# Optimization experiments

Measured on AMD Instinct MI355X. Metric: run time of the kernel, lower is better.

The kernel has to match this reference:

```python
import jax, jax.numpy as jnp
import numpy as np
import math

B, N, D_IN, D_OUT = 8, 2048, 128, 128
NEG_BIG = -10000.0

def setup_inputs() -> dict:
    key = jax.random.key(0)
    k_in, k_adj, kq, kk, kv, kbq, kbk, kbv = jax.random.split(key, 8)
    scale = 1.0 / math.sqrt(D_IN)
    inputs = jax.random.normal(k_in, (B, N, D_IN), dtype=jnp.float32)
    adj = jax.random.randint(k_adj, (B, N, N), 0, 2, dtype=jnp.int32)
    Wq = jax.random.uniform(kq, (D_IN, D_OUT), jnp.float32, -scale, scale)
    Wk = jax.random.uniform(kk, (D_IN, D_OUT), jnp.float32, -scale, scale)
    Wv = jax.random.uniform(kv, (D_IN, D_OUT), jnp.float32, -scale, scale)
    bq = jax.random.uniform(kbq, (D_OUT,), jnp.float32, -scale, scale)
    bk = jax.random.uniform(kbk, (D_OUT,), jnp.float32, -scale, scale)
    bv = jax.random.uniform(kbv, (D_OUT,), jnp.float32, -scale, scale)
    return {"inputs": inputs, "adj": adj, "Wq": Wq, "bq": bq,
            "Wk": Wk, "bk": bk, "Wv": Wv, "bv": bv}

def reference(inputs, adj, Wq, bq, Wk, bk, Wv, bv):
    # QKV projections: [B, N, D_OUT]
    q = inputs @ Wq + bq
    k = inputs @ Wk + bk
    v = inputs @ Wv + bv
    # additive adjacency bias: 0 where edge, -10000 where no edge
    bias = (1.0 - adj.astype(jnp.float32)) * NEG_BIG
    # scaled dot-product scores [B, N, N]
    a = jnp.einsum('bnd,bmd->bnm', q, k) / jnp.sqrt(jnp.float32(q.shape[-1]))
    a = a + bias
    p = jax.nn.softmax(a, axis=-1)  # dropout_prob=0.0 -> identity
    h = jnp.einsum('bnm,bmd->bnd', p, v)
    return jax.nn.elu(h)
```

## Files before the change

### kernel.cpp

```cpp
#include <hip/hip_runtime.h>

typedef unsigned short u16;
typedef __bf16 bf16x8 __attribute__((ext_vector_type(8)));
typedef float  fx4    __attribute__((ext_vector_type(4)));

__device__ __forceinline__ u16 f2bf(float f) {
    unsigned int x = __builtin_bit_cast(unsigned int, f);
    x = x + 0x7fffu + ((x >> 16) & 1u);
    return (u16)(x >> 16);
}
__device__ __forceinline__ __bf16 f2bf16(float f) {
    return __builtin_bit_cast(__bf16, f2bf(f));
}
__device__ __forceinline__ u16 f2bf_fast(float f) {
    return __builtin_bit_cast(u16, (__bf16)f);
}
__device__ __forceinline__ float exp2_fast(float x) {
#if __has_builtin(__builtin_amdgcn_exp2f)
    return __builtin_amdgcn_exp2f(x);
#else
    float r;
    __asm__ volatile("v_exp_f32 %0, %1" : "=v"(r) : "v"(x));
    return r;
#endif
}
__device__ __forceinline__ int ld_nt(const int* p) {
    return __builtin_nontemporal_load(p);
}

#define MFMA16(a, b, c) __builtin_amdgcn_mfma_f32_16x16x32_bf16((a), (b), (c), 0, 0, 0)
#define WAVE_LDS_SYNC() __asm__ volatile("s_waitcnt lgkmcnt(0)" ::: "memory")

__global__ __launch_bounds__(256) void wt_kernel(
    const float* __restrict__ Wq, const float* __restrict__ Wk,
    const float* __restrict__ Wv, u16* __restrict__ WT)
{
    const int o = blockIdx.x * 256 + threadIdx.x;
    const int p = o >> 14, rem = o & 16383, c = rem >> 7, k = rem & 127;
    const float* W = (p == 0) ? Wq : ((p == 1) ? Wk : Wv);
    WT[o] = f2bf(W[k * 128 + c]);
}

__global__ __launch_bounds__(256, 2) void qkv_kernel(
    const float* __restrict__ X, const u16* __restrict__ WT,
    const float* __restrict__ bq, const float* __restrict__ bk,
    const float* __restrict__ bv,
    u16* __restrict__ Qf, u16* __restrict__ Kf, u16* __restrict__ Vf)
{
    __shared__ __align__(16) u16 st[4][1024];

    const int tid  = threadIdx.x;
    const int w    = tid >> 6;
    const int lane = tid & 63;
    const int n    = lane & 15;
    const int quad = lane >> 4;
    const int gw   = blockIdx.x * 4 + w;
    const int rt   = gw >> 1, ch = gw & 1;
    const int row0 = rt * 16;
    const int b    = row0 >> 11;
    const int keyb = row0 & 2047;

    u16* sw = st[w];

    bf16x8 af[4];
    {
        const float* xr = X + (size_t)(row0 + n) * 128;
#pragma unroll
        for (int kk = 0; kk < 4; ++kk) {
            float4 f0 = *(const float4*)(xr + kk * 32 + quad * 8);
            float4 f1 = *(const float4*)(xr + kk * 32 + quad * 8 + 4);
            bf16x8 a;
            a[0] = f2bf16(f0.x); a[1] = f2bf16(f0.y); a[2] = f2bf16(f0.z); a[3] = f2bf16(f0.w);
            a[4] = f2bf16(f1.x); a[5] = f2bf16(f1.y); a[6] = f2bf16(f1.z); a[7] = f2bf16(f1.w);
            af[kk] = a;
        }
    }

    const float* Bs[2] = {bq, bk};
#pragma unroll
    for (int p = 0; p < 2; ++p) {
        const u16* wt = WT + p * 16384;
#pragma unroll
        for (int nt = 0; nt < 4; ++nt) {
            const int col0 = ch * 64 + nt * 16;
            fx4 acc = {0.f, 0.f, 0.f, 0.f};
#pragma unroll
            for (int kk = 0; kk < 4; ++kk) {
                bf16x8 bf = __builtin_bit_cast(bf16x8,
                    *(const uint4*)&wt[(col0 + n) * 128 + kk * 32 + quad * 8]);
                acc = MFMA16(af[kk], bf, acc);
            }
            const float bb = Bs[p][col0 + n];
            const int c = col0 + n;
            const int li = ((c >> 5) & 1) * 512 + ((c >> 3) & 3) * 128 + (c & 7);
#pragma unroll
            for (int r = 0; r < 4; ++r)
                sw[li + (quad * 4 + r) * 8] = f2bf(acc[r] + bb);
        }
        WAVE_LDS_SYNC();
        u16* gbase;
        if (p == 0) {
            gbase = Qf + (((size_t)(b * 128 + (keyb >> 4)) * 4 + 2 * ch) << 9);
        } else {
            gbase = Kf + (((size_t)((b * 64 + (keyb >> 5)) * 2 + ((keyb >> 4) & 1)) * 4 + 2 * ch) << 9);
        }
        *(uint4*)(gbase + lane * 8)       = *(const uint4*)(sw + lane * 8);
        *(uint4*)(gbase + 512 + lane * 8) = *(const uint4*)(sw + 512 + lane * 8);
    }

    {
        const u16* wtv = WT + 2 * 16384;
        const int hk    = (keyb >> 4) & 1;
        const int vtile = keyb >> 5;
#pragma unroll
        for (int d0 = 0; d0 < 4; ++d0) {
            const int dbase = ch * 64 + d0 * 16;
            fx4 acc = {0.f, 0.f, 0.f, 0.f};
#pragma unroll
            for (int kk = 0; kk < 4; ++kk) {
                bf16x8 wf = __builtin_bit_cast(bf16x8,
                    *(const uint4*)&wtv[(dbase + n) * 128 + kk * 32 + quad * 8]);
                acc = MFMA16(wf, af[kk], acc);
            }
            const int li = d0 * 256 + ((n >> 3) & 1) * 128 + (n & 7);
#pragma unroll
            for (int r = 0; r < 4; ++r)
                sw[li + (quad * 4 + r) * 8] = f2bf(acc[r] + bv[dbase + quad * 4 + r]);
        }
        WAVE_LDS_SYNC();
        const int l5 = lane >> 5, lo = lane & 31;
#pragma unroll
        for (int i = 0; i < 2; ++i) {
            const int c2 = l5 + 2 * i;
            u16* g = Vf + (((size_t)(b * 64 + vtile) * 8 + ch * 4 + c2) << 9)
                        + hk * 256 + lo * 8;
            *(uint4*)g = *(const uint4*)(sw + c2 * 256 + lo * 8);
        }
    }
}

__global__ __launch_bounds__(256, 3) void attn_kernel(
    const u16* __restrict__ Qf, const u16* __restrict__ Kf,
    const u16* __restrict__ Vf, const int* __restrict__ adj,
    float* __restrict__ out)
{
    __shared__ __align__(16) float mO[4][16 * 128];
    __shared__ __align__(16) float ml[4][16];
    __shared__ __align__(16) u16 pl[4][640];

    const int tid  = threadIdx.x;
    const int h    = tid >> 6;
    const int lane = tid & 63;
    const int n    = lane & 15;
    const int quad = lane >> 4;
    const int b    = blockIdx.x & 7;
    const int qt   = blockIdx.x >> 3;
    const int q0   = qt * 16;
    const size_t bN = (size_t)b * 2048;

    bf16x8 qf[4];
    {
        const u16* qp = Qf + ((size_t)(b * 128 + qt) << 11) + lane * 8;
#pragma unroll
        for (int kk = 0; kk < 4; ++kk)
            qf[kk] = __builtin_bit_cast(bf16x8, *(const uint4*)(qp + (kk << 9)));
    }
    const u16* Kb = Kf + ((size_t)b << 18);
    const u16* Vb = Vf + ((size_t)b << 18);

    fx4 O[8];
#pragma unroll
    for (int i = 0; i < 8; ++i) O[i] = (fx4){0.f, 0.f, 0.f, 0.f};
    fx4 Lacc = {0.f, 0.f, 0.f, 0.f};

    bf16x8 ONESF;
    {
        const __bf16 one = __builtin_bit_cast(__bf16, (u16)0x3F80);
#pragma unroll
        for (int j = 0; j < 8; ++j) ONESF[j] = one;
    }

    const int* adjb = adj + (bN + q0 + quad * 4) * 2048;
    const float C2 = 0.12751742f;
    const float MB = -14427.0f;
    u16* pw = pl[h];

    float b0c[4], b1c[4];
    {
        const int k0 = h * 512;
#pragma unroll
        for (int r = 0; r < 4; ++r) {
            b0c[r] = ld_nt(&adjb[(size_t)r * 2048 + k0 + n])      ? 0.f : MB;
            b1c[r] = ld_nt(&adjb[(size_t)r * 2048 + k0 + 16 + n]) ? 0.f : MB;
        }
    }

    for (int t = 0; t < 16; ++t) {
        const int tg = h * 16 + t;
        const u16* kt_ = Kb + ((size_t)tg << 12) + lane * 8;
        const u16* vt_ = Vb + ((size_t)tg << 12) + lane * 8;

        bf16x8 kb[8];
#pragma unroll
        for (int kk = 0; kk < 8; ++kk)
            kb[kk] = __builtin_bit_cast(bf16x8, *(const uint4*)(kt_ + (kk << 9)));

        bf16x8 vf[8];
#pragma unroll
        for (int dt = 0; dt < 8; ++dt)
            vf[dt] = __builtin_bit_cast(bf16x8, *(const uint4*)(vt_ + (dt << 9)));

        float b0n[4], b1n[4];
        if (t < 15) {
            const int kn = h * 512 + (t + 1) * 32;
#pragma unroll
            for (int r = 0; r < 4; ++r) {
                b0n[r] = ld_nt(&adjb[(size_t)r * 2048 + kn + n])      ? 0.f : MB;
                b1n[r] = ld_nt(&adjb[(size_t)r * 2048 + kn + 16 + n]) ? 0.f : MB;
            }
        }

        fx4 S0 = {0.f, 0.f, 0.f, 0.f}, S1 = {0.f, 0.f, 0.f, 0.f};
#pragma unroll
        for (int kk = 0; kk < 4; ++kk) {
            S0 = MFMA16(qf[kk], kb[kk], S0);
            S1 = MFMA16(qf[kk], kb[4 + kk], S1);
        }

#pragma unroll
        for (int r = 0; r < 4; ++r) {
            const float e0 = exp2_fast(__builtin_fmaf(S0[r], C2, b0c[r]));
            const float e1 = exp2_fast(__builtin_fmaf(S1[r], C2, b1c[r]));
            pw[(quad * 4 + r) * 40 + n]      = f2bf_fast(e0);
            pw[(quad * 4 + r) * 40 + 16 + n] = f2bf_fast(e1);
        }

        WAVE_LDS_SYNC();
        bf16x8 pf = __builtin_bit_cast(bf16x8, *(const uint4*)&pw[n * 40 + quad * 8]);

#pragma unroll
        for (int dt = 0; dt < 8; ++dt)
            O[dt] = MFMA16(pf, vf[dt], O[dt]);
        Lacc = MFMA16(pf, ONESF, Lacc);

#pragma unroll
        for (int r = 0; r < 4; ++r) { b0c[r] = b0n[r]; b1c[r] = b1n[r]; }
    }

#pragma unroll
    for (int r = 0; r < 4; ++r) {
        const int row = quad * 4 + r;
        if (n == 0) ml[h][row] = Lacc[r];
#pragma unroll
        for (int dt = 0; dt < 8; ++dt)
            mO[h][row * 128 + dt * 16 + n] = O[dt][r];
    }
    __syncthreads();

#pragma unroll
    for (int r = 0; r < 4; ++r) {
        const int row = quad * 4 + r;
        const float L = ml[0][row] + ml[1][row] + ml[2][row] + ml[3][row];
        const float linv = 1.f / L;
        float* po = out + (bN + q0 + row) * 128;
#pragma unroll
        for (int dti = 0; dti < 2; ++dti) {
            const int dt = h * 2 + dti;
            float o = 0.f;
#pragma unroll
            for (int g = 0; g < 4; ++g) o += mO[g][row * 128 + dt * 16 + n];
            const float hh = o * linv;
            po[dt * 16 + n] = (hh > 0.f) ? hh : (__expf(hh) - 1.f);
        }
    }
}

extern "C" void kernel_launch(void* const* d_in, const int* in_sizes, int n_in,
                              void* d_out, int out_size, void* d_ws, size_t ws_size,
                              hipStream_t stream) {
    (void)in_sizes; (void)n_in; (void)out_size; (void)ws_size;
    const float* X   = (const float*)d_in[0];
    const int*   adj = (const int*)d_in[1];
    const float* Wq  = (const float*)d_in[2];
    const float* bq  = (const float*)d_in[3];
    const float* Wk  = (const float*)d_in[4];
    const float* bk  = (const float*)d_in[5];
    const float* Wv  = (const float*)d_in[6];
    const float* bv  = (const float*)d_in[7];
    float* out = (float*)d_out;

    u16* WT  = (u16*)d_out;
    u16* Qf  = (u16*)d_ws;
    u16* Kf  = Qf + (size_t)16384 * 128;
    u16* Vf  = Kf + (size_t)16384 * 128;

    wt_kernel<<<192, 256, 0, stream>>>(Wq, Wk, Wv, WT);
    qkv_kernel<<<512, 256, 0, stream>>>(X, WT, bq, bk, bv, Qf, Kf, Vf);
    attn_kernel<<<1024, 256, 0, stream>>>(Qf, Kf, Vf, adj, out);
}
```

Before: 302.8 us.

## Pre-pack adjacency into bitmask kernel and read bits in attention

Adds a pack kernel that uses wave ballots to compress the int32 adjacency matrix into a 64-bit-per-64-entries bitmask in workspace. The attention kernel then loads one 32-bit mask word per row per tile instead of 32 int32 values, and raises its occupancy launch bound from 3 to 4. The adjacency still has to be read once in full by the pack kernel, so the main saving is fewer loads and less register pressure inside the attention loop, at the cost of an extra launch and a small mask write and read.

```diff
diff --git a/kernel.cpp b/kernel.cpp
--- a/kernel.cpp
+++ b/kernel.cpp
@@ -1,6 +1,8 @@
 #include <hip/hip_runtime.h>
 
 typedef unsigned short u16;
+typedef unsigned int   u32;
+typedef unsigned long long u64;
 typedef __bf16 bf16x8 __attribute__((ext_vector_type(8)));
 typedef float  fx4    __attribute__((ext_vector_type(4)));
 
@@ -39,6 +41,25 @@
     const int p = o >> 14, rem = o & 16383, c = rem >> 7, k = rem & 127;
     const float* W = (p == 0) ? Wq : ((p == 1) ? Wk : Wv);
     WT[o] = f2bf(W[k * 128 + c]);
+}
+
+__global__ __launch_bounds__(256) void pack_kernel(
+    const int* __restrict__ adj, u64* __restrict__ mask64)
+{
+    const int w = threadIdx.x >> 6, lane = threadIdx.x & 63;
+    const int gw = blockIdx.x * 4 + w;
+    const int nw = gridDim.x * 4;
+    for (int it = gw; it < 131072; it += nw) {
+        const int* base = adj + (size_t)it * 256 + lane;
+        const u64 b0 = __ballot(ld_nt(base +   0) != 0);
+        const u64 b1 = __ballot(ld_nt(base +  64) != 0);
+        const u64 b2 = __ballot(ld_nt(base + 128) != 0);
+        const u64 b3 = __ballot(ld_nt(base + 192) != 0);
+        if (lane < 4) {
+            const u64 v = (lane == 0) ? b0 : (lane == 1) ? b1 : (lane == 2) ? b2 : b3;
+            mask64[(size_t)it * 4 + lane] = v;
+        }
+    }
 }
 
 __global__ __launch_bounds__(256, 2) void qkv_kernel(
@@ -139,9 +160,9 @@
     }
 }
 
-__global__ __launch_bounds__(256, 3) void attn_kernel(
+__global__ __launch_bounds__(256, 4) void attn_kernel(
     const u16* __restrict__ Qf, const u16* __restrict__ Kf,
-    const u16* __restrict__ Vf, const int* __restrict__ adj,
+    const u16* __restrict__ Vf, const u32* __restrict__ mask,
     float* __restrict__ out)
 {
     __shared__ __align__(16) float mO[4][16 * 128];
@@ -180,20 +201,14 @@
         for (int j = 0; j < 8; ++j) ONESF[j] = one;
     }
 
-    const int* adjb = adj + (bN + q0 + quad * 4) * 2048;
+    const u32* mrow = mask + (bN + q0 + quad * 4) * 64 + h * 16;
     const float C2 = 0.12751742f;
     const float MB = -14427.0f;
     u16* pw = pl[h];
 
-    float b0c[4], b1c[4];
-    {
-        const int k0 = h * 512;
-#pragma unroll
-        for (int r = 0; r < 4; ++r) {
-            b0c[r] = ld_nt(&adjb[(size_t)r * 2048 + k0 + n])      ? 0.f : MB;
-            b1c[r] = ld_nt(&adjb[(size_t)r * 2048 + k0 + 16 + n]) ? 0.f : MB;
-        }
-    }
+    u32 mc[4];
+#pragma unroll
+    for (int r = 0; r < 4; ++r) mc[r] = mrow[r * 64];
 
     for (int t = 0; t < 16; ++t) {
         const int tg = h * 16 + t;
@@ -210,14 +225,10 @@
         for (int dt = 0; dt < 8; ++dt)
             vf[dt] = __builtin_bit_cast(bf16x8, *(const uint4*)(vt_ + (dt << 9)));
 
-        float b0n[4], b1n[4];
+        u32 mn_[4];
         if (t < 15) {
-            const int kn = h * 512 + (t + 1) * 32;
-#pragma unroll
-            for (int r = 0; r < 4; ++r) {
-                b0n[r] = ld_nt(&adjb[(size_t)r * 2048 + kn + n])      ? 0.f : MB;
-                b1n[r] = ld_nt(&adjb[(size_t)r * 2048 + kn + 16 + n]) ? 0.f : MB;
-            }
+#pragma unroll
+            for (int r = 0; r < 4; ++r) mn_[r] = mrow[r * 64 + t + 1];
         }
 
         fx4 S0 = {0.f, 0.f, 0.f, 0.f}, S1 = {0.f, 0.f, 0.f, 0.f};
@@ -229,8 +240,10 @@
 
 #pragma unroll
         for (int r = 0; r < 4; ++r) {
-            const float e0 = exp2_fast(__builtin_fmaf(S0[r], C2, b0c[r]));
-            const float e1 = exp2_fast(__builtin_fmaf(S1[r], C2, b1c[r]));
+            const float bias0 = ((mc[r] >> n) & 1u)        ? 0.f : MB;
+            const float bias1 = ((mc[r] >> (16 + n)) & 1u) ? 0.f : MB;
+            const float e0 = exp2_fast(__builtin_fmaf(S0[r], C2, bias0));
+            const float e1 = exp2_fast(__builtin_fmaf(S1[r], C2, bias1));
             pw[(quad * 4 + r) * 40 + n]      = f2bf_fast(e0);
             pw[(quad * 4 + r) * 40 + 16 + n] = f2bf_fast(e1);
         }
@@ -244,7 +257,7 @@
         Lacc = MFMA16(pf, ONESF, Lacc);
 
 #pragma unroll
-        for (int r = 0; r < 4; ++r) { b0c[r] = b0n[r]; b1c[r] = b1n[r]; }
+        for (int r = 0; r < 4; ++r) mc[r] = mn_[r];
     }
 
 #pragma unroll
@@ -289,12 +302,14 @@
     const float* bv  = (const float*)d_in[7];
     float* out = (float*)d_out;
 
-    u16* WT  = (u16*)d_out;
-    u16* Qf  = (u16*)d_ws;
-    u16* Kf  = Qf + (size_t)16384 * 128;
-    u16* Vf  = Kf + (size_t)16384 * 128;
+    u16* WT   = (u16*)d_out;
+    u16* Qf   = (u16*)d_ws;
+    u16* Kf   = Qf + (size_t)16384 * 128;
+    u16* Vf   = Kf + (size_t)16384 * 128;
+    u32* mask = (u32*)(Vf + (size_t)16384 * 128);
 
     wt_kernel<<<192, 256, 0, stream>>>(Wq, Wk, Wv, WT);
     qkv_kernel<<<512, 256, 0, stream>>>(X, WT, bq, bk, bv, Qf, Kf, Vf);
-    attn_kernel<<<1024, 256, 0, stream>>>(Qf, Kf, Vf, adj, out);
-}
+    pack_kernel<<<2048, 256, 0, stream>>>(adj, (u64*)mask);
+    attn_kernel<<<1024, 256, 0, stream>>>(Qf, Kf, Vf, mask, out);
+}
```

After: 255.1 us. -15.8%, faster.
